# Kernel optimization log

Measured on AMD Instinct MI355X. Metric: run time of the kernel, lower is better.

## Reference

```python
import jax, jax.numpy as jnp
import numpy as np

EPS = 1e-5
INF = 1e5


def setup_inputs() -> dict:
    key = jax.random.key(0)
    ks = iter(jax.random.split(key, 32))
    B, N, F, H, NH, C = 2, 384, 64, 64, 4, 32
    def lin(k, fi, fo):
        return jax.random.normal(k, (fi, fo), jnp.float32) / np.sqrt(fi).astype(np.float32)
    d = {}
    d['h'] = jax.random.normal(next(ks), (B, N, F), jnp.float32)
    d['x'] = jax.random.normal(next(ks), (B, N, 3), jnp.float32)
    # edge_model (ConcatenationFilter): Linear(2F+1,H), SiLU, Linear(H,H), SiLU
    d['We0'] = lin(next(ks), 2 * F + 1, H); d['be0'] = jnp.zeros(H, jnp.float32)
    d['We1'] = lin(next(ks), H, H);         d['be1'] = jnp.zeros(H, jnp.float32)
    # semantic_attention_mlp: Linear(H, n_heads), LeakyReLU(0.2)
    d['Ws'] = lin(next(ks), H, NH);         d['bs'] = jnp.zeros(NH, jnp.float32)
    # coefficients_mlp: Linear(H,H), SiLU, Linear(H,C)
    d['Wc0'] = lin(next(ks), H, H);         d['bc0'] = jnp.zeros(H, jnp.float32)
    d['Wc1'] = lin(next(ks), H, C);         d['bc1'] = jnp.zeros(C, jnp.float32)
    # post_norm_mlp: Linear(C,H), SiLU, Linear(H,H)
    d['Wp0'] = lin(next(ks), C, H);         d['bp0'] = jnp.zeros(H, jnp.float32)
    d['Wp1'] = lin(next(ks), H, H);         d['bp1'] = jnp.zeros(H, jnp.float32)
    # coordinate_mlp: Linear(H,H), SiLU, Linear(H,1,bias=False) init gain 1e-3
    d['Wx0'] = lin(next(ks), H, H);         d['bx0'] = jnp.zeros(H, jnp.float32)
    d['Wx1'] = lin(next(ks), H, 1) * 1e-3
    # node_mlp: Linear(NH*H + H + F, H), SiLU, Linear(H, F)
    d['Wn0'] = lin(next(ks), NH * H + H + F, H); d['bn0'] = jnp.zeros(H, jnp.float32)
    d['Wn1'] = lin(next(ks), H, F);         d['bn1'] = jnp.zeros(F, jnp.float32)
    d['log_gamma'] = jnp.zeros(NH, jnp.float32)
    return d


def _forward(h, x, We0, be0, We1, be1, Ws, bs, Wc0, bc0, Wc1, bc1,
             Wp0, bp0, Wp1, bp1, Wx0, bx0, Wx1, Wn0, bn0, Wn1, bn1, log_gamma):
    B, N, F = h.shape
    silu = jax.nn.silu

    # pairwise displacements and distances: (B,N,N,3), (B,N,N,1)
    x_minus_xt = x[:, :, None, :] - x[:, None, :, :]
    norm = jnp.sqrt(jnp.sum(x_minus_xt * x_minus_xt, axis=-1, keepdims=True) + EPS)

    # pairwise node-feature concat + distance -> edge MLP (ConcatenationFilter)
    hi = jnp.broadcast_to(h[:, :, None, :], (B, N, N, F))
    hj = jnp.broadcast_to(h[:, None, :, :], (B, N, N, F))
    e_in = jnp.concatenate([hi, hj, norm], axis=-1)           # (B,N,N,2F+1)
    h_e = silu(silu(e_in @ We0 + be0) @ We1 + be1)            # (B,N,N,H)

    eye = jnp.eye(N, dtype=h.dtype)[None, :, :, None]         # mask self-edges

    # euclidean attention per head, softmax over neighbors j (axis=-2)
    eu = jax.nn.softmax(-(norm + INF * eye) * jnp.exp(log_gamma), axis=-2)  # (B,N,N,NH)
    # semantic attention
    sem_logits = jax.nn.leaky_relu(h_e @ Ws + bs, 0.2) - INF * eye
    sem = jax.nn.softmax(sem_logits, axis=-2)                 # (B,N,N,NH)
    comb = eu * sem
    comb = comb / (jnp.sum(comb, axis=-2, keepdims=True) + EPS)

    # attention-weighted multi-head edge features, aggregated over neighbors
    h_e_att = (comb[..., :, None] * h_e[..., None, :]).reshape(B, N, N, -1)  # (B,N,N,NH*H)
    h_e_agg = jnp.sum(h_e_att, axis=-2)                       # (B,N,NH*H)

    # spatial attention: equivariant combinations of unit direction vectors
    coeff = silu(h_e @ Wc0 + bc0) @ Wc1 + bc1                 # (B,N,N,C)
    x_hat = x_minus_xt / (norm + EPS)                         # (B,N,N,3)
    combinations = coeff[..., :, None] * x_hat[..., None, :]  # (B,N,N,C,3)
    comb_sum = jnp.mean(combinations, axis=2)                 # mean over j -> (B,N,C,3)
    comb_norm = jnp.sum(comb_sum * comb_sum, axis=-1)         # (B,N,C)
    h_comb = silu(comb_norm @ Wp0 + bp0) @ Wp1 + bp1          # (B,N,H)

    # node update (residual)
    node_in = jnp.concatenate([h, h_e_agg, h_comb], axis=-1)
    h_out = h + (silu(node_in @ Wn0 + bn0) @ Wn1 + bn1)

    # coordinate update: scalar-gated displacements, mean over neighbors
    scale = silu(h_e @ Wx0 + bx0) @ Wx1                       # (B,N,N,1)
    x_out = x + jnp.mean(x_minus_xt * scale, axis=2)          # (B,N,3)
    return h_out, x_out


def reference(h, x, We0, be0, We1, be1, Ws, bs, Wc0, bc0, Wc1, bc1,
              Wp0, bp0, Wp1, bp1, Wx0, bx0, Wx1, Wn0, bn0, Wn1, bn1, log_gamma):
    return _forward(h, x, We0, be0, We1, be1, Ws, bs, Wc0, bc0, Wc1, bc1,
                    Wp0, bp0, Wp1, bp1, Wx0, bx0, Wx1, Wn0, bn0, Wn1, bn1, log_gamma)
```

## Files before the change

kernel.cpp:

```cpp
#include <hip/hip_runtime.h>

#define NPT 384
#define NB 2
#define NROW (NB*NPT)
#define NT 6
#define HOFF 49152
#define RECB 1024
#define REC_OFF 424960

typedef unsigned short u16;
typedef unsigned int u32;
typedef __bf16 bf16x8 __attribute__((ext_vector_type(8)));
typedef float f32x4 __attribute__((ext_vector_type(4)));

struct alignas(16) U4 { u32 x, y, z, w; };

constexpr float kEPS = 1e-5f;
constexpr float kINF = 1e5f;

__device__ __forceinline__ u16 f2b(float f) { __bf16 b = (__bf16)f; return __builtin_bit_cast(u16, b); }
__device__ __forceinline__ u32 pk2(float lo, float hi) { return (u32)f2b(lo) | ((u32)f2b(hi) << 16); }
__device__ __forceinline__ float b2f(u32 u) { return __uint_as_float(u << 16); }
__device__ __forceinline__ float silu_f(float v) { return v * __builtin_amdgcn_rcpf(1.f + __expf(-v)); }

__global__ __launch_bounds__(64) void sake_prep(
    const float* __restrict__ h, const float* __restrict__ We0,
    const float* __restrict__ be0, const float* __restrict__ We1,
    const float* __restrict__ Wc0, const float* __restrict__ Wc1,
    const float* __restrict__ Wx0, const float* __restrict__ Ws,
    float* __restrict__ U, float* __restrict__ V, u16* __restrict__ WT)
{
  const int t = threadIdx.x;
  const int blk = blockIdx.x;
  if (blk < NROW) {
    __shared__ float hs[64];
    hs[t] = h[blk * 64 + t];
    __syncthreads();
    float u = be0[t], v = 0.f;
#pragma unroll 8
    for (int k = 0; k < 64; k++) {
      float hv = hs[k];
      u = fmaf(hv, We0[k * 64 + t], u);
      v = fmaf(hv, We0[(64 + k) * 64 + t], v);
    }
    U[blk * 64 + t] = u;
    V[blk * 64 + t] = v;
  } else {
    const int wsel = blk - NROW;
    if (wsel == 4) {
      u16* dst = WT + 14336;
      for (int o = t; o < 16 * 64; o += 64) {
        int c = o >> 6, k = o & 63;
        dst[o] = (c < 4) ? f2b(Ws[k * 4 + c]) : (u16)0;
      }
      return;
    }
    const float* src; int nout; u16* dst;
    if      (wsel == 0) { src = We1; nout = 64; dst = WT;         }
    else if (wsel == 1) { src = Wc0; nout = 64; dst = WT + 4096;  }
    else if (wsel == 2) { src = Wx0; nout = 64; dst = WT + 8192;  }
    else                { src = Wc1; nout = 32; dst = WT + 12288; }
    const int total = 64 * nout;
    for (int o = t; o < total; o += 64) {
      int n = o >> 6, k = o & 63;
      dst[o] = f2b(src[k * nout + n]);
    }
  }
}

struct MainArgs {
  const float *x, *U, *V;
  const u16 *We1T, *Wc0T, *Wx0T, *Wc1T, *WsPT;
  const float *We0, *bs, *be1, *bc0, *bc1, *bx0, *Wx1, *log_gamma;
  char* rec;
};

__device__ __forceinline__ void readB(const u16* tile, int j, int kg, bf16x8& f0, bf16x8& f1) {
  const int r7 = j & 7;
  f0 = *(const bf16x8*)(tile + j * 64 + ((kg ^ r7) << 3));
  f1 = *(const bf16x8*)(tile + j * 64 + (((kg + 4) ^ r7) << 3));
}

template<int NNT, bool SILU_, int NCH, bool DUALT>
__device__ __forceinline__ void gemmT8(const u16* __restrict__ wG, const float* __restrict__ biasG,
                                       bf16x8 bf0, bf16x8 bf1, u16* out, u16* oTT,
                                       int j, int kg, int l15, int nbase)
{
  const int jm = j & (NCH - 1);
#pragma unroll
  for (int nt = 0; nt < NNT; nt++) {
    const int nrow = nbase + (nt << 4) + l15;
    bf16x8 a0 = *(const bf16x8*)(wG + nrow * 64 + (kg << 3));
    bf16x8 a1 = *(const bf16x8*)(wG + nrow * 64 + 32 + (kg << 3));
    f32x4 acc = {0.f, 0.f, 0.f, 0.f};
    acc = __builtin_amdgcn_mfma_f32_16x16x32_bf16(a0, bf0, acc, 0, 0, 0);
    acc = __builtin_amdgcn_mfma_f32_16x16x32_bf16(a1, bf1, acc, 0, 0, 0);
    const int n0 = nbase + (nt << 4) + (kg << 2);
    const float4 bv = *(const float4*)(biasG + n0);
    float s0, s1, s2, s3;
    if constexpr (SILU_) {
      s0 = silu_f(acc[0] + bv.x); s1 = silu_f(acc[1] + bv.y);
      s2 = silu_f(acc[2] + bv.z); s3 = silu_f(acc[3] + bv.w);
    } else {
      s0 = acc[0] + bv.x; s1 = acc[1] + bv.y;
      s2 = acc[2] + bv.z; s3 = acc[3] + bv.w;
    }
    const u16 q0 = f2b(s0), q1 = f2b(s1), q2 = f2b(s2), q3 = f2b(s3);
    u32 pkx = (u32)q0 | ((u32)q1 << 16), pky = (u32)q2 | ((u32)q3 << 16);
    const int c = n0 >> 3;
    u32* dst = (u32*)(out + j * (NCH * 8) + (((c ^ jm) << 3) + (n0 & 7)));
    dst[0] = pkx; dst[1] = pky;
    if constexpr (DUALT) {
      const int jq = (j >> 3), j7 = j & 7;
      const u16 qs[4] = {q0, q1, q2, q3};
#pragma unroll
      for (int r = 0; r < 4; r++) {
        const int f = n0 + r;
        oTT[f * 64 + ((jq ^ (f & 7)) << 3) + j7] = qs[r];
      }
    }
  }
}

__global__ __launch_bounds__(512, 8) void sake_main(MainArgs A)
{
  __shared__ __align__(16) u16 buf0[64 * 64];
  __shared__ __align__(16) u16 hes[64 * 64];
  __shared__ __align__(16) u16 hesT[64 * 64];
  __shared__ __align__(16) u16 coeff[64 * 32];
  __shared__ __align__(16) u16 E_lds[16 * 64];
  __shared__ float raw_lds[64 * 5];
  __shared__ float disp[64][3];
  __shared__ float nrm_s[64], invn_s[64];

  const int t = threadIdx.x;
  const int w = t >> 6, lane = t & 63;
  const int kg = lane >> 4, l15 = lane & 15;
  const int bt = blockIdx.x;
  const int i = bt % NPT;
  const int bj = bt / NPT;
  const int jt = bj % NT, b = bj / NT;
  const int bi = b * NPT + i;
  const int j0 = jt << 6;
  char* rec = A.rec + (size_t)(bi * NT + jt) * RECB;

  const int jj3 = t >> 3, q8 = t & 7;
  {
    const int jrow = j0 + jj3;
    const float* xp = &A.x[(b * NPT + jrow) * 3];
    const float xj0 = xp[0], xj1 = xp[1], xj2 = xp[2];
    const float xi0 = A.x[bi * 3 + 0], xi1 = A.x[bi * 3 + 1], xi2 = A.x[bi * 3 + 2];
    const float4* vp = (const float4*)(A.V + (size_t)(b * NPT + jrow) * 64 + q8 * 8);
    const float4 v0_ = vp[0], v1_ = vp[1];
    const float4* Up = (const float4*)(A.U + bi * 64 + q8 * 8);
    const float4 u0_ = Up[0], u1_ = Up[1];
    const float4* Wd = (const float4*)(A.We0 + 128 * 64 + q8 * 8);
    const float4 w0_ = Wd[0], w1_ = Wd[1];
    float dx0 = xi0 - xj0, dx1 = xi1 - xj1, dx2 = xi2 - xj2;
    float nr = sqrtf(fmaf(dx0, dx0, fmaf(dx1, dx1, fmaf(dx2, dx2, kEPS))));
    if (q8 == 0) {
      disp[jj3][0] = dx0; disp[jj3][1] = dx1; disp[jj3][2] = dx2;
      nrm_s[jj3] = nr; invn_s[jj3] = __builtin_amdgcn_rcpf(nr + kEPS);
    }
    float vv[8] = {v0_.x, v0_.y, v0_.z, v0_.w, v1_.x, v1_.y, v1_.z, v1_.w};
    float uu[8] = {u0_.x, u0_.y, u0_.z, u0_.w, u1_.x, u1_.y, u1_.z, u1_.w};
    float ww[8] = {w0_.x, w0_.y, w0_.z, w0_.w, w1_.x, w1_.y, w1_.z, w1_.w};
    float sv[8];
#pragma unroll
    for (int e = 0; e < 8; e++) sv[e] = silu_f(uu[e] + vv[e] + nr * ww[e]);
    U4 u4;
    u4.x = pk2(sv[0], sv[1]); u4.y = pk2(sv[2], sv[3]);
    u4.z = pk2(sv[4], sv[5]); u4.w = pk2(sv[6], sv[7]);
    *(U4*)(buf0 + jj3 * 64 + ((q8 ^ (jj3 & 7)) << 3)) = u4;
  }
  __syncthreads();

  {
    const int rs = w >> 1, ch = w & 1;
    const int jr = (rs << 4) + l15;
    bf16x8 bh0, bh1;
    readB(buf0, jr, kg, bh0, bh1);
    gemmT8<2, true, 8, true>(A.We1T, A.be1, bh0, bh1, hes, hesT, jr, kg, l15, ch << 5);
  }
  __syncthreads();

  const int stripe = w & 3;
  const int jrow16 = (stripe << 4) + l15;

  float xA0 = 0, xA1 = 0, xA2 = 0;
  {
    bf16x8 he0, he1;
    readB(hes, jrow16, kg, he0, he1);
    if (w < 4) {
      gemmT8<4, true, 8, false>(A.Wc0T, A.bc0, he0, he1, buf0, nullptr, jrow16, kg, l15, 0);
    } else {
      float sacc = 0.f;
#pragma unroll
      for (int nt = 0; nt < 4; nt++) {
        const int nrow = (nt << 4) + l15;
        bf16x8 a0 = *(const bf16x8*)(A.Wx0T + nrow * 64 + (kg << 3));
        bf16x8 a1 = *(const bf16x8*)(A.Wx0T + nrow * 64 + 32 + (kg << 3));
        f32x4 acc = {0.f, 0.f, 0.f, 0.f};
        acc = __builtin_amdgcn_mfma_f32_16x16x32_bf16(a0, he0, acc, 0, 0, 0);
        acc = __builtin_amdgcn_mfma_f32_16x16x32_bf16(a1, he1, acc, 0, 0, 0);
        const int n0 = (nt << 4) + (kg << 2);
        const float4 bv = *(const float4*)(A.bx0 + n0);
        const float4 wx = *(const float4*)(A.Wx1 + n0);
        sacc = fmaf(silu_f(acc[0] + bv.x), wx.x, sacc);
        sacc = fmaf(silu_f(acc[1] + bv.y), wx.y, sacc);
        sacc = fmaf(silu_f(acc[2] + bv.z), wx.z, sacc);
        sacc = fmaf(silu_f(acc[3] + bv.w), wx.w, sacc);
      }
      sacc += __shfl_xor(sacc, 16, 64);
      sacc += __shfl_xor(sacc, 32, 64);
      if (kg == 0) {
        xA0 = disp[jrow16][0] * sacc;
        xA1 = disp[jrow16][1] * sacc;
        xA2 = disp[jrow16][2] * sacc;
      }
    }
  }
  __syncthreads();

  if (w < 4) {
    bf16x8 c10, c11;
    readB(buf0, jrow16, kg, c10, c11);
    gemmT8<2, false, 4, false>(A.Wc1T, A.bc1, c10, c11, coeff, nullptr, jrow16, kg, l15, 0);
  } else {
    const int m0 = stripe << 4;
    const int arow = m0 + l15;
    const int r7a = arow & 7;
    bf16x8 a0 = *(const bf16x8*)(hes + arow * 64 + ((kg ^ r7a) << 3));
    bf16x8 a1 = *(const bf16x8*)(hes + arow * 64 + (((kg + 4) ^ r7a) << 3));
    const u16* wrow = A.WsPT + l15 * 64;
    bf16x8 b0 = *(const bf16x8*)(wrow + (kg << 3));
    bf16x8 b1 = *(const bf16x8*)(wrow + 32 + (kg << 3));
    f32x4 acc = {0.f, 0.f, 0.f, 0.f};
    acc = __builtin_amdgcn_mfma_f32_16x16x32_bf16(a0, b0, acc, 0, 0, 0);
    acc = __builtin_amdgcn_mfma_f32_16x16x32_bf16(a1, b1, acc, 0, 0, 0);
    if (l15 < 4) {
#pragma unroll
      for (int r = 0; r < 4; r++)
        raw_lds[(m0 + (kg << 2) + r) * 5 + l15] = acc[r];
    }
  }
  __syncthreads();

  float cA0 = 0, cA1 = 0, cA2 = 0;
  if (w < 4) {
    const int jj = lane, head = w;
    float raw = raw_lds[jj * 5 + head] + A.bs[head];
    float bsem = (raw > 0.f) ? raw : 0.2f * raw;
    const bool self = (j0 + jj) == i;
    if (self) bsem -= kINF;
    const float gam = __expf(A.log_gamma[head]);
    const float aeu = -(nrm_s[jj] + (self ? kINF : 0.f)) * gam;
    const float eL = __expf(aeu + bsem);
    const float eB = __expf(bsem);
    const float eA = __expf(aeu);
    float sL = eL, sB = eB, sA = eA;
#pragma unroll
    for (int m = 32; m >= 1; m >>= 1) {
      sL += __shfl_xor(sL, m, 64);
      sB += __shfl_xor(sB, m, 64);
      sA += __shfl_xor(sA, m, 64);
    }
    E_lds[head * 64 + (((jj >> 3) ^ head) << 3) + (jj & 7)] = f2b(eL);
    if (lane == 0) {
      float* sp = (float*)(rec + 908) + head * 5;
      sp[0] = 0.f; sp[1] = sL; sp[2] = 0.f; sp[3] = sB; sp[4] = sA;
    }
  } else {
    const int tp = t - 256;
    const int c = tp & 31, g = tp >> 5;
    const int cc = c >> 3, ce = c & 7;
#pragma unroll
    for (int it = 0; it < 8; ++it) {
      const int jj = (g << 3) + it;
      const float s = b2f(coeff[jj * 32 + ((cc ^ (jj & 3)) << 3) + ce]) * invn_s[jj];
      cA0 = fmaf(s, disp[jj][0], cA0);
      cA1 = fmaf(s, disp[jj][1], cA1);
      cA2 = fmaf(s, disp[jj][2], cA2);
    }
  }
  __syncthreads();

  float* cascr = (float*)buf0;
  float* xscr = (float*)raw_lds;
  if (w < 4) {
    const int erow = l15;
    const int e7 = erow & 7;
    bf16x8 ea0 = *(const bf16x8*)(E_lds + erow * 64 + ((kg ^ e7) << 3));
    bf16x8 ea1 = *(const bf16x8*)(E_lds + erow * 64 + (((kg + 4) ^ e7) << 3));
    const int f = (w << 4) + l15;
    const int f7 = f & 7;
    bf16x8 hb0 = *(const bf16x8*)(hesT + f * 64 + ((kg ^ f7) << 3));
    bf16x8 hb1 = *(const bf16x8*)(hesT + f * 64 + (((kg + 4) ^ f7) << 3));
    f32x4 aF = {0.f, 0.f, 0.f, 0.f};
    aF = __builtin_amdgcn_mfma_f32_16x16x32_bf16(ea0, hb0, aF, 0, 0, 0);
    aF = __builtin_amdgcn_mfma_f32_16x16x32_bf16(ea1, hb1, aF, 0, 0, 0);
    if (kg == 0) {
      u16* rA = (u16*)rec;
#pragma unroll
      for (int r = 0; r < 4; r++) rA[r * 64 + f] = f2b(aF[r]);
    }
  } else {
    const int tp = t - 256;
    cascr[tp * 3 + 0] = cA0; cascr[tp * 3 + 1] = cA1; cascr[tp * 3 + 2] = cA2;
    if (kg == 0) {
      xscr[jrow16 * 3 + 0] = xA0; xscr[jrow16 * 3 + 1] = xA1; xscr[jrow16 * 3 + 2] = xA2;
    }
  }
  __syncthreads();

  if (t < 96) {
    const int c = t & 31, d = t >> 5;
    float s = 0.f;
#pragma unroll
    for (int g = 0; g < 8; g++) s += cascr[(g * 32 + c) * 3 + d];
    ((float*)(rec + 512))[d * 32 + c] = s;
  } else if (t < 99) {
    const int d = t - 96;
    float s = 0.f;
    for (int k = 0; k < 64; k++) s += xscr[k * 3 + d];
    ((float*)(rec + 896))[d] = s;
  }
}

struct MergeArgs {
  const float *h, *x, *Wp0, *bp0, *Wp1, *bp1, *Wn0, *bn0, *Wn1, *bn1;
  const char* rec;
  float* out;
};

__global__ __launch_bounds__(256) void sake_merge(MergeArgs M)
{
  __shared__ float sc[NT][20];
  __shared__ float wAl[NT][4];
  __shared__ float coefh[4];
  __shared__ float node_in[384];
  __shared__ float cmv[96];
  __shared__ float nrm32[32];
  __shared__ float t0s[64];
  __shared__ float scr[256];

  const int t = threadIdx.x;
  const int bi = blockIdx.x;
  const char* rb = M.rec + (size_t)bi * NT * RECB;

  if (t < NT * 20) {
    const int tt = t / 20, k = t % 20;
    sc[tt][k] = ((const float*)(rb + tt * RECB + 908))[k];
  }
  if (t < 64) node_in[t] = M.h[bi * 64 + t];
  __syncthreads();
  if (t < 4) {
    const int hh = t;
    float mL = -1e30f, mb = -1e30f;
    for (int tt = 0; tt < NT; tt++) {
      mL = fmaxf(mL, sc[tt][hh * 5 + 0]);
      mb = fmaxf(mb, sc[tt][hh * 5 + 2]);
    }
    float SL = 0.f, Sb = 0.f, Sa = 0.f;
    for (int tt = 0; tt < NT; tt++) {
      const float wa = __expf(sc[tt][hh * 5 + 0] - mL);
      wAl[tt][hh] = wa;
      SL = fmaf(wa, sc[tt][hh * 5 + 1], SL);
      Sb = fmaf(__expf(sc[tt][hh * 5 + 2] - mb), sc[tt][hh * 5 + 3], Sb);
      Sa += sc[tt][hh * 5 + 4];
    }
    const float Ff = __expf(mL - mb);
    coefh[hh] = Ff / fmaf(SL, Ff, kEPS * Sa * Sb);
  }
  __syncthreads();
  {
    const int hh = t >> 6, f = t & 63;
    float s = 0.f;
#pragma unroll
    for (int tt = 0; tt < NT; tt++)
      s = fmaf(wAl[tt][hh], b2f(((const u16*)(rb + tt * RECB))[hh * 64 + f]), s);
    node_in[64 + hh * 64 + f] = s * coefh[hh];
  }
  if (t < 96) {
    float s = 0.f;
#pragma unroll
    for (int tt = 0; tt < NT; tt++) s += ((const float*)(rb + tt * RECB + 512))[t];
    cmv[t] = s * (1.f / 384.f);
  }
  if (t >= 128 && t < 131) {
    const int d = t - 128;
    float s = 0.f;
#pragma unroll
    for (int tt = 0; tt < NT; tt++) s += ((const float*)(rb + tt * RECB + 896))[d];
    M.out[HOFF + bi * 3 + d] = M.x[bi * 3 + d] + s * (1.f / 384.f);
  }
  __syncthreads();
  if (t < 32) {
    const float v0 = cmv[t], v1 = cmv[32 + t], v2 = cmv[64 + t];
    nrm32[t] = v0 * v0 + v1 * v1 + v2 * v2;
  }
  __syncthreads();
  if (t < 64) {
    float a = M.bp0[t];
    for (int c = 0; c < 32; c++) a = fmaf(nrm32[c], M.Wp0[c * 64 + t], a);
    t0s[t] = silu_f(a);
  }
  __syncthreads();
  if (t < 64) {
    float a = M.bp1[t];
    for (int k = 0; k < 64; k++) a = fmaf(t0s[k], M.Wp1[k * 64 + t], a);
    node_in[320 + t] = a;
  }
  __syncthreads();
  {
    const int f = t & 63, q = t >> 6;
    float a = 0.f;
    const int k0 = q * 96;
    for (int k = 0; k < 96; k++) a = fmaf(node_in[k0 + k], M.Wn0[(k0 + k) * 64 + f], a);
    scr[t] = a;
  }
  __syncthreads();
  if (t < 64) {
    const float s = scr[t] + scr[64 + t] + scr[128 + t] + scr[192 + t] + M.bn0[t];
    t0s[t] = silu_f(s);
  }
  __syncthreads();
  if (t < 64) {
    float a = M.bn1[t];
    for (int k = 0; k < 64; k++) a = fmaf(t0s[k], M.Wn1[k * 64 + t], a);
    M.out[bi * 64 + t] = M.h[bi * 64 + t] + a;
  }
}

extern "C" void kernel_launch(void* const* d_in, const int* in_sizes, int n_in,
                              void* d_out, int out_size, void* d_ws, size_t ws_size,
                              hipStream_t stream)
{
  (void)in_sizes; (void)n_in; (void)out_size; (void)ws_size;
  const float* h   = (const float*)d_in[0];
  const float* x   = (const float*)d_in[1];
  const float* We0 = (const float*)d_in[2];
  const float* be0 = (const float*)d_in[3];
  const float* We1 = (const float*)d_in[4];
  const float* be1 = (const float*)d_in[5];
  const float* Ws  = (const float*)d_in[6];
  const float* bs  = (const float*)d_in[7];
  const float* Wc0 = (const float*)d_in[8];
  const float* bc0 = (const float*)d_in[9];
  const float* Wc1 = (const float*)d_in[10];
  const float* bc1 = (const float*)d_in[11];
  const float* Wp0 = (const float*)d_in[12];
  const float* bp0 = (const float*)d_in[13];
  const float* Wp1 = (const float*)d_in[14];
  const float* bp1 = (const float*)d_in[15];
  const float* Wx0 = (const float*)d_in[16];
  const float* bx0 = (const float*)d_in[17];
  const float* Wx1 = (const float*)d_in[18];
  const float* Wn0 = (const float*)d_in[19];
  const float* bn0 = (const float*)d_in[20];
  const float* Wn1 = (const float*)d_in[21];
  const float* bn1 = (const float*)d_in[22];
  const float* lg  = (const float*)d_in[23];

  float* U = (float*)d_ws;
  float* V = U + NROW * 64;
  u16* WT = (u16*)(V + NROW * 64);
  char* rec = (char*)d_ws + REC_OFF;

  sake_prep<<<NROW + 5, 64, 0, stream>>>(h, We0, be0, We1, Wc0, Wc1, Wx0, Ws, U, V, WT);

  MainArgs A;
  A.x = x; A.U = U; A.V = V;
  A.We1T = WT; A.Wc0T = WT + 4096; A.Wx0T = WT + 8192; A.Wc1T = WT + 12288;
  A.WsPT = WT + 14336;
  A.We0 = We0; A.bs = bs; A.be1 = be1; A.bc0 = bc0; A.bc1 = bc1;
  A.bx0 = bx0; A.Wx1 = Wx1; A.log_gamma = lg;
  A.rec = rec;
  sake_main<<<NROW * NT, 512, 0, stream>>>(A);

  MergeArgs Mg;
  Mg.h = h; Mg.x = x;
  Mg.Wp0 = Wp0; Mg.bp0 = bp0; Mg.Wp1 = Wp1; Mg.bp1 = bp1;
  Mg.Wn0 = Wn0; Mg.bn0 = bn0; Mg.Wn1 = Wn1; Mg.bn1 = bn1;
  Mg.rec = rec; Mg.out = (float*)d_out;
  sake_merge<<<NROW, 256, 0, stream>>>(Mg);
}
```

Measured before the change: 100.7 us.

## Give each wave its own 16-row stripe and drop most block barriers

Shrinks the main edge kernel from 512 to 256 threads per block. Each wave now owns one 16-row stripe of the j-tile and runs all the per-edge MLP stages for it, where before the work was split between two wave groups. Because every wave only reads rows it wrote itself, most block-wide barriers become per-wave LDS waitcnt fences, and the shared E buffer and inverse-norm array are folded into existing scratch. The aim is less barrier stalling and fewer idle waves; the cost is more serial work per wave and different occupancy.

```diff
diff --git a/kernel.cpp b/kernel.cpp
--- a/kernel.cpp
+++ b/kernel.cpp
@@ -17,6 +17,8 @@
 
 constexpr float kEPS = 1e-5f;
 constexpr float kINF = 1e5f;
+
+#define WAVE_LDS_FENCE() asm volatile("s_waitcnt lgkmcnt(0)" ::: "memory")
 
 __device__ __forceinline__ u16 f2b(float f) { __bf16 b = (__bf16)f; return __builtin_bit_cast(u16, b); }
 __device__ __forceinline__ u32 pk2(float lo, float hi) { return (u32)f2b(lo) | ((u32)f2b(hi) << 16); }
@@ -122,16 +124,16 @@
   }
 }
 
-__global__ __launch_bounds__(512, 8) void sake_main(MainArgs A)
+__global__ __launch_bounds__(256, 4) void sake_main(MainArgs A)
 {
   __shared__ __align__(16) u16 buf0[64 * 64];
   __shared__ __align__(16) u16 hes[64 * 64];
   __shared__ __align__(16) u16 hesT[64 * 64];
   __shared__ __align__(16) u16 coeff[64 * 32];
-  __shared__ __align__(16) u16 E_lds[16 * 64];
   __shared__ float raw_lds[64 * 5];
   __shared__ float disp[64][3];
-  __shared__ float nrm_s[64], invn_s[64];
+  __shared__ float nrm_s[64];
+  __shared__ float xstash[64 * 3];
 
   const int t = threadIdx.x;
   const int w = t >> 6, lane = t & 63;
@@ -144,94 +146,86 @@
   const int j0 = jt << 6;
   char* rec = A.rec + (size_t)(bi * NT + jt) * RECB;
 
-  const int jj3 = t >> 3, q8 = t & 7;
-  {
-    const int jrow = j0 + jj3;
-    const float* xp = &A.x[(b * NPT + jrow) * 3];
+  const int jrow = (w << 4) + l15;
+
+  const int jj2 = t >> 2, q4 = t & 3;
+  {
+    const int jr = j0 + jj2;
+    const float* xp = &A.x[(b * NPT + jr) * 3];
     const float xj0 = xp[0], xj1 = xp[1], xj2 = xp[2];
     const float xi0 = A.x[bi * 3 + 0], xi1 = A.x[bi * 3 + 1], xi2 = A.x[bi * 3 + 2];
-    const float4* vp = (const float4*)(A.V + (size_t)(b * NPT + jrow) * 64 + q8 * 8);
-    const float4 v0_ = vp[0], v1_ = vp[1];
-    const float4* Up = (const float4*)(A.U + bi * 64 + q8 * 8);
-    const float4 u0_ = Up[0], u1_ = Up[1];
-    const float4* Wd = (const float4*)(A.We0 + 128 * 64 + q8 * 8);
-    const float4 w0_ = Wd[0], w1_ = Wd[1];
+    const float4* vp = (const float4*)(A.V + (size_t)(b * NPT + jr) * 64 + q4 * 16);
+    const float4 v0_ = vp[0], v1_ = vp[1], v2_ = vp[2], v3_ = vp[3];
+    const float4* Up = (const float4*)(A.U + bi * 64 + q4 * 16);
+    const float4 u0_ = Up[0], u1_ = Up[1], u2_ = Up[2], u3_ = Up[3];
+    const float4* Wd = (const float4*)(A.We0 + 128 * 64 + q4 * 16);
+    const float4 w0_ = Wd[0], w1_ = Wd[1], w2_ = Wd[2], w3_ = Wd[3];
     float dx0 = xi0 - xj0, dx1 = xi1 - xj1, dx2 = xi2 - xj2;
     float nr = sqrtf(fmaf(dx0, dx0, fmaf(dx1, dx1, fmaf(dx2, dx2, kEPS))));
-    if (q8 == 0) {
-      disp[jj3][0] = dx0; disp[jj3][1] = dx1; disp[jj3][2] = dx2;
-      nrm_s[jj3] = nr; invn_s[jj3] = __builtin_amdgcn_rcpf(nr + kEPS);
-    }
-    float vv[8] = {v0_.x, v0_.y, v0_.z, v0_.w, v1_.x, v1_.y, v1_.z, v1_.w};
-    float uu[8] = {u0_.x, u0_.y, u0_.z, u0_.w, u1_.x, u1_.y, u1_.z, u1_.w};
-    float ww[8] = {w0_.x, w0_.y, w0_.z, w0_.w, w1_.x, w1_.y, w1_.z, w1_.w};
-    float sv[8];
-#pragma unroll
-    for (int e = 0; e < 8; e++) sv[e] = silu_f(uu[e] + vv[e] + nr * ww[e]);
-    U4 u4;
-    u4.x = pk2(sv[0], sv[1]); u4.y = pk2(sv[2], sv[3]);
-    u4.z = pk2(sv[4], sv[5]); u4.w = pk2(sv[6], sv[7]);
-    *(U4*)(buf0 + jj3 * 64 + ((q8 ^ (jj3 & 7)) << 3)) = u4;
-  }
-  __syncthreads();
-
-  {
-    const int rs = w >> 1, ch = w & 1;
-    const int jr = (rs << 4) + l15;
+    if (q4 == 0) { disp[jj2][0] = dx0; disp[jj2][1] = dx1; disp[jj2][2] = dx2; nrm_s[jj2] = nr; }
+    float vv[16] = {v0_.x, v0_.y, v0_.z, v0_.w, v1_.x, v1_.y, v1_.z, v1_.w,
+                    v2_.x, v2_.y, v2_.z, v2_.w, v3_.x, v3_.y, v3_.z, v3_.w};
+    float uu[16] = {u0_.x, u0_.y, u0_.z, u0_.w, u1_.x, u1_.y, u1_.z, u1_.w,
+                    u2_.x, u2_.y, u2_.z, u2_.w, u3_.x, u3_.y, u3_.z, u3_.w};
+    float ww[16] = {w0_.x, w0_.y, w0_.z, w0_.w, w1_.x, w1_.y, w1_.z, w1_.w,
+                    w2_.x, w2_.y, w2_.z, w2_.w, w3_.x, w3_.y, w3_.z, w3_.w};
+    float sv[16];
+#pragma unroll
+    for (int e = 0; e < 16; e++) sv[e] = silu_f(uu[e] + vv[e] + nr * ww[e]);
+    U4 lo, hi;
+    lo.x = pk2(sv[0], sv[1]);   lo.y = pk2(sv[2], sv[3]);
+    lo.z = pk2(sv[4], sv[5]);   lo.w = pk2(sv[6], sv[7]);
+    hi.x = pk2(sv[8], sv[9]);   hi.y = pk2(sv[10], sv[11]);
+    hi.z = pk2(sv[12], sv[13]); hi.w = pk2(sv[14], sv[15]);
+    const int r7 = jj2 & 7;
+    *(U4*)(buf0 + jj2 * 64 + (((q4 * 2) ^ r7) << 3)) = lo;
+    *(U4*)(buf0 + jj2 * 64 + (((q4 * 2 + 1) ^ r7) << 3)) = hi;
+  }
+  WAVE_LDS_FENCE();
+
+  {
     bf16x8 bh0, bh1;
-    readB(buf0, jr, kg, bh0, bh1);
-    gemmT8<2, true, 8, true>(A.We1T, A.be1, bh0, bh1, hes, hesT, jr, kg, l15, ch << 5);
-  }
-  __syncthreads();
-
-  const int stripe = w & 3;
-  const int jrow16 = (stripe << 4) + l15;
-
-  float xA0 = 0, xA1 = 0, xA2 = 0;
-  {
-    bf16x8 he0, he1;
-    readB(hes, jrow16, kg, he0, he1);
-    if (w < 4) {
-      gemmT8<4, true, 8, false>(A.Wc0T, A.bc0, he0, he1, buf0, nullptr, jrow16, kg, l15, 0);
-    } else {
-      float sacc = 0.f;
-#pragma unroll
-      for (int nt = 0; nt < 4; nt++) {
-        const int nrow = (nt << 4) + l15;
-        bf16x8 a0 = *(const bf16x8*)(A.Wx0T + nrow * 64 + (kg << 3));
-        bf16x8 a1 = *(const bf16x8*)(A.Wx0T + nrow * 64 + 32 + (kg << 3));
-        f32x4 acc = {0.f, 0.f, 0.f, 0.f};
-        acc = __builtin_amdgcn_mfma_f32_16x16x32_bf16(a0, he0, acc, 0, 0, 0);
-        acc = __builtin_amdgcn_mfma_f32_16x16x32_bf16(a1, he1, acc, 0, 0, 0);
-        const int n0 = (nt << 4) + (kg << 2);
-        const float4 bv = *(const float4*)(A.bx0 + n0);
-        const float4 wx = *(const float4*)(A.Wx1 + n0);
-        sacc = fmaf(silu_f(acc[0] + bv.x), wx.x, sacc);
-        sacc = fmaf(silu_f(acc[1] + bv.y), wx.y, sacc);
-        sacc = fmaf(silu_f(acc[2] + bv.z), wx.z, sacc);
-        sacc = fmaf(silu_f(acc[3] + bv.w), wx.w, sacc);
-      }
-      sacc += __shfl_xor(sacc, 16, 64);
-      sacc += __shfl_xor(sacc, 32, 64);
-      if (kg == 0) {
-        xA0 = disp[jrow16][0] * sacc;
-        xA1 = disp[jrow16][1] * sacc;
-        xA2 = disp[jrow16][2] * sacc;
-      }
-    }
-  }
-  __syncthreads();
-
-  if (w < 4) {
-    bf16x8 c10, c11;
-    readB(buf0, jrow16, kg, c10, c11);
-    gemmT8<2, false, 4, false>(A.Wc1T, A.bc1, c10, c11, coeff, nullptr, jrow16, kg, l15, 0);
-  } else {
-    const int m0 = stripe << 4;
-    const int arow = m0 + l15;
-    const int r7a = arow & 7;
-    bf16x8 a0 = *(const bf16x8*)(hes + arow * 64 + ((kg ^ r7a) << 3));
-    bf16x8 a1 = *(const bf16x8*)(hes + arow * 64 + (((kg + 4) ^ r7a) << 3));
+    readB(buf0, jrow, kg, bh0, bh1);
+    gemmT8<4, true, 8, true>(A.We1T, A.be1, bh0, bh1, hes, hesT, jrow, kg, l15, 0);
+  }
+  WAVE_LDS_FENCE();
+
+  bf16x8 he0, he1;
+  readB(hes, jrow, kg, he0, he1);
+
+  gemmT8<4, true, 8, false>(A.Wc0T, A.bc0, he0, he1, buf0, nullptr, jrow, kg, l15, 0);
+
+  {
+    float sacc = 0.f;
+#pragma unroll
+    for (int nt = 0; nt < 4; nt++) {
+      const int nrow = (nt << 4) + l15;
+      bf16x8 a0 = *(const bf16x8*)(A.Wx0T + nrow * 64 + (kg << 3));
+      bf16x8 a1 = *(const bf16x8*)(A.Wx0T + nrow * 64 + 32 + (kg << 3));
+      f32x4 acc = {0.f, 0.f, 0.f, 0.f};
+      acc = __builtin_amdgcn_mfma_f32_16x16x32_bf16(a0, he0, acc, 0, 0, 0);
+      acc = __builtin_amdgcn_mfma_f32_16x16x32_bf16(a1, he1, acc, 0, 0, 0);
+      const int n0 = (nt << 4) + (kg << 2);
+      const float4 bv = *(const float4*)(A.bx0 + n0);
+      const float4 wx = *(const float4*)(A.Wx1 + n0);
+      sacc = fmaf(silu_f(acc[0] + bv.x), wx.x, sacc);
+      sacc = fmaf(silu_f(acc[1] + bv.y), wx.y, sacc);
+      sacc = fmaf(silu_f(acc[2] + bv.z), wx.z, sacc);
+      sacc = fmaf(silu_f(acc[3] + bv.w), wx.w, sacc);
+    }
+    sacc += __shfl_xor(sacc, 16, 64);
+    sacc += __shfl_xor(sacc, 32, 64);
+    if (kg == 0) {
+      xstash[jrow * 3 + 0] = disp[jrow][0] * sacc;
+      xstash[jrow * 3 + 1] = disp[jrow][1] * sacc;
+      xstash[jrow * 3 + 2] = disp[jrow][2] * sacc;
+    }
+  }
+
+  {
+    const int r7a = jrow & 7;
+    bf16x8 a0 = *(const bf16x8*)(hes + jrow * 64 + ((kg ^ r7a) << 3));
+    bf16x8 a1 = *(const bf16x8*)(hes + jrow * 64 + (((kg + 4) ^ r7a) << 3));
     const u16* wrow = A.WsPT + l15 * 64;
     bf16x8 b0 = *(const bf16x8*)(wrow + (kg << 3));
     bf16x8 b1 = *(const bf16x8*)(wrow + 32 + (kg << 3));
@@ -239,15 +233,24 @@
     acc = __builtin_amdgcn_mfma_f32_16x16x32_bf16(a0, b0, acc, 0, 0, 0);
     acc = __builtin_amdgcn_mfma_f32_16x16x32_bf16(a1, b1, acc, 0, 0, 0);
     if (l15 < 4) {
+      const int m0 = w << 4;
 #pragma unroll
       for (int r = 0; r < 4; r++)
         raw_lds[(m0 + (kg << 2) + r) * 5 + l15] = acc[r];
     }
   }
+  WAVE_LDS_FENCE();
+
+  {
+    bf16x8 c10, c11;
+    readB(buf0, jrow, kg, c10, c11);
+    gemmT8<2, false, 4, false>(A.Wc1T, A.bc1, c10, c11, coeff, nullptr, jrow, kg, l15, 0);
+  }
+
   __syncthreads();
 
   float cA0 = 0, cA1 = 0, cA2 = 0;
-  if (w < 4) {
+  {
     const int jj = lane, head = w;
     float raw = raw_lds[jj * 5 + head] + A.bs[head];
     float bsem = (raw > 0.f) ? raw : 0.2f * raw;
@@ -265,33 +268,39 @@
       sB += __shfl_xor(sB, m, 64);
       sA += __shfl_xor(sA, m, 64);
     }
-    E_lds[head * 64 + (((jj >> 3) ^ head) << 3) + (jj & 7)] = f2b(eL);
+    u16* E = buf0 + 3072;
+    E[head * 64 + (((jj >> 3) ^ head) << 3) + (jj & 7)] = f2b(eL);
     if (lane == 0) {
       float* sp = (float*)(rec + 908) + head * 5;
       sp[0] = 0.f; sp[1] = sL; sp[2] = 0.f; sp[3] = sB; sp[4] = sA;
     }
-  } else {
-    const int tp = t - 256;
-    const int c = tp & 31, g = tp >> 5;
+  }
+  {
+    const int c = t & 31, g = t >> 5;
     const int cc = c >> 3, ce = c & 7;
 #pragma unroll
     for (int it = 0; it < 8; ++it) {
       const int jj = (g << 3) + it;
-      const float s = b2f(coeff[jj * 32 + ((cc ^ (jj & 3)) << 3) + ce]) * invn_s[jj];
+      const float s = b2f(coeff[jj * 32 + ((cc ^ (jj & 3)) << 3) + ce]) *
+                      __builtin_amdgcn_rcpf(nrm_s[jj] + kEPS);
       cA0 = fmaf(s, disp[jj][0], cA0);
       cA1 = fmaf(s, disp[jj][1], cA1);
       cA2 = fmaf(s, disp[jj][2], cA2);
     }
   }
-  __syncthreads();
-
-  float* cascr = (float*)buf0;
-  float* xscr = (float*)raw_lds;
-  if (w < 4) {
+  {
+    float* cascr = (float*)buf0;
+    cascr[t * 3 + 0] = cA0; cascr[t * 3 + 1] = cA1; cascr[t * 3 + 2] = cA2;
+  }
+
+  __syncthreads();
+
+  {
+    const u16* E = buf0 + 3072;
     const int erow = l15;
     const int e7 = erow & 7;
-    bf16x8 ea0 = *(const bf16x8*)(E_lds + erow * 64 + ((kg ^ e7) << 3));
-    bf16x8 ea1 = *(const bf16x8*)(E_lds + erow * 64 + (((kg + 4) ^ e7) << 3));
+    bf16x8 ea0 = *(const bf16x8*)(E + erow * 64 + ((kg ^ e7) << 3));
+    bf16x8 ea1 = *(const bf16x8*)(E + erow * 64 + (((kg + 4) ^ e7) << 3));
     const int f = (w << 4) + l15;
     const int f7 = f & 7;
     bf16x8 hb0 = *(const bf16x8*)(hesT + f * 64 + ((kg ^ f7) << 3));
@@ -304,26 +313,21 @@
 #pragma unroll
       for (int r = 0; r < 4; r++) rA[r * 64 + f] = f2b(aF[r]);
     }
-  } else {
-    const int tp = t - 256;
-    cascr[tp * 3 + 0] = cA0; cascr[tp * 3 + 1] = cA1; cascr[tp * 3 + 2] = cA2;
-    if (kg == 0) {
-      xscr[jrow16 * 3 + 0] = xA0; xscr[jrow16 * 3 + 1] = xA1; xscr[jrow16 * 3 + 2] = xA2;
-    }
-  }
-  __syncthreads();
-
-  if (t < 96) {
-    const int c = t & 31, d = t >> 5;
-    float s = 0.f;
-#pragma unroll
-    for (int g = 0; g < 8; g++) s += cascr[(g * 32 + c) * 3 + d];
-    ((float*)(rec + 512))[d * 32 + c] = s;
-  } else if (t < 99) {
-    const int d = t - 96;
-    float s = 0.f;
-    for (int k = 0; k < 64; k++) s += xscr[k * 3 + d];
-    ((float*)(rec + 896))[d] = s;
+  }
+  {
+    const float* cascr = (const float*)buf0;
+    if (t < 96) {
+      const int c = t & 31, d = t >> 5;
+      float s = 0.f;
+#pragma unroll
+      for (int g = 0; g < 8; g++) s += cascr[(g * 32 + c) * 3 + d];
+      ((float*)(rec + 512))[d * 32 + c] = s;
+    } else if (t < 99) {
+      const int d = t - 96;
+      float s = 0.f;
+      for (int k = 0; k < 64; k++) s += xstash[k * 3 + d];
+      ((float*)(rec + 896))[d] = s;
+    }
   }
 }
 
@@ -476,7 +480,7 @@
   A.We0 = We0; A.bs = bs; A.be1 = be1; A.bc0 = bc0; A.bc1 = bc1;
   A.bx0 = bx0; A.Wx1 = Wx1; A.log_gamma = lg;
   A.rec = rec;
-  sake_main<<<NROW * NT, 512, 0, stream>>>(A);
+  sake_main<<<NROW * NT, 256, 0, stream>>>(A);
 
   MergeArgs Mg;
   Mg.h = h; Mg.x = x;
```

After: 102.1 us. Within noise of the previous version (+1.4%).
